# Kernel tuning notes

Hardware: AMD Instinct MI355X
Metric: run time of the kernel (lower is better)

The kernel has to match this reference:

```python
import jax, jax.numpy as jnp
import numpy as np

N, E, P, D = 100000, 800000, 100000, 128

def setup_inputs() -> dict:
    key = jax.random.key(0)
    ks = jax.random.split(key, 24)
    def w(k, i, o):
        return jax.random.normal(k, (i, o), jnp.float32) * (1.0 / np.sqrt(i))
    inp = {
        'x': jax.random.normal(ks[0], (N, D), jnp.float32),
        'src': jax.random.randint(ks[1], (E,), 0, N, jnp.int32),
        'dst': jax.random.randint(ks[2], (E,), 0, N, jnp.int32),
        'pos_src': jax.random.randint(ks[3], (P,), 0, N, jnp.int32),
        'pos_dst': jax.random.randint(ks[4], (P,), 0, N, jnp.int32),
        'neg_src': jax.random.randint(ks[5], (P,), 0, N, jnp.int32),
        'neg_dst': jax.random.randint(ks[6], (P,), 0, N, jnp.int32),
        # SAGEConv params: fc_self, fc_neigh (+bias) per layer
        'Ws0': w(ks[7], D, D), 'Wn0': w(ks[8], D, D), 'b0': jnp.zeros((D,), jnp.float32),
        'Ws1': w(ks[9], D, D), 'Wn1': w(ks[10], D, D), 'b1': jnp.zeros((D,), jnp.float32),
        'Ws2': w(ks[11], D, D), 'Wn2': w(ks[12], D, D), 'b2': jnp.zeros((D,), jnp.float32),
        # predictor MLP: D->D->D->2
        'Wp0': w(ks[13], D, D), 'bp0': jnp.zeros((D,), jnp.float32),
        'Wp1': w(ks[14], D, D), 'bp1': jnp.zeros((D,), jnp.float32),
        'Wp2': w(ks[15], D, 2), 'bp2': jnp.zeros((2,), jnp.float32),
    }
    return inp

def _sage_layer(h, src, dst, n, Ws, Wn, b, act):
    # mean aggregation over in-neighbors (gather -> segment_sum -> divide)
    msum = jax.ops.segment_sum(h[src], dst, num_segments=n)      # [N, D]
    deg = jax.ops.segment_sum(jnp.ones_like(dst, jnp.float32), dst, num_segments=n)
    h_neigh = msum / jnp.maximum(deg, 1.0)[:, None]
    out = h @ Ws + h_neigh @ Wn + b
    return jax.nn.relu(out) if act else out

def _predict(hs, hd, Wp0, bp0, Wp1, bp1, Wp2, bp2):
    z = hs * hd
    z = jax.nn.relu(z @ Wp0 + bp0)
    z = jax.nn.relu(z @ Wp1 + bp1)
    return jax.nn.softmax(z @ Wp2 + bp2, axis=1)[:, 1]

def reference(x, src, dst, pos_src, pos_dst, neg_src, neg_dst,
              Ws0, Wn0, b0, Ws1, Wn1, b1, Ws2, Wn2, b2,
              Wp0, bp0, Wp1, bp1, Wp2, bp2):
    n = x.shape[0]
    h = _sage_layer(x, src, dst, n, Ws0, Wn0, b0, True)
    h = _sage_layer(h, src, dst, n, Ws1, Wn1, b1, True)
    h = _sage_layer(h, src, dst, n, Ws2, Wn2, b2, False)
    pos = _predict(h[pos_src], h[pos_dst], Wp0, bp0, Wp1, bp1, Wp2, bp2)
    neg = _predict(h[neg_src], h[neg_dst], Wp0, bp0, Wp1, bp1, Wp2, bp2)
    return (pos, neg)
```

## Files before the change

kernel.cpp:

```cpp
#include <hip/hip_runtime.h>
#include <cstdint>
#include <cstddef>
#include <cmath>

#define D 128

typedef short bf16x8 __attribute__((ext_vector_type(8)));
typedef float f32x4 __attribute__((ext_vector_type(4)));

__device__ __forceinline__ ushort f2b(float f) {
  uint x = __float_as_uint(f);
  uint r = ((x >> 16) & 1u) + 0x7fffu;
  return (ushort)((x + r) >> 16);
}
__device__ __forceinline__ float b2f(ushort u) {
  return __uint_as_float(((uint)u) << 16);
}

__global__ __launch_bounds__(256) void k_degree_p(const int* __restrict__ dst, int E,
    int* __restrict__ deg, float scale, int CE) {
  int part = blockIdx.x & 7, chunk = blockIdx.x >> 3;
  long base = (long)chunk * CE;
  for (int i = threadIdx.x; i < CE; i += 256) {
    long e = base + i;
    if (e < E) {
      int d = dst[e];
      int p = (int)((float)d * scale); if (p > 7) p = 7;
      if (p == part) atomicAdd(&deg[d], 1);
    }
  }
}

__global__ __launch_bounds__(256) void k_fill_p(const int* __restrict__ src,
    const int* __restrict__ dst, int E, int* __restrict__ cursor,
    int* __restrict__ csrc, float scale, int CE) {
  int part = blockIdx.x & 7, chunk = blockIdx.x >> 3;
  long base = (long)chunk * CE;
  for (int i = threadIdx.x; i < CE; i += 256) {
    long e = base + i;
    if (e < E) {
      int d = dst[e];
      int p = (int)((float)d * scale); if (p > 7) p = 7;
      if (p == part) {
        int s = src[e];
        int pos = atomicAdd(&cursor[d], 1);
        csrc[pos] = s;
      }
    }
  }
}

#define SCAN_T 256
#define SCAN_E 4
#define SCAN_CHUNK (SCAN_T * SCAN_E)

__global__ void k_scan_partial(const int* __restrict__ deg, int n, int* __restrict__ part) {
  __shared__ int s[SCAN_T];
  int base = blockIdx.x * SCAN_CHUNK;
  int sum = 0;
  for (int i = 0; i < SCAN_E; ++i) {
    int idx = base + (int)threadIdx.x * SCAN_E + i;
    if (idx < n) sum += deg[idx];
  }
  s[threadIdx.x] = sum; __syncthreads();
  for (int ofs = SCAN_T / 2; ofs > 0; ofs >>= 1) {
    if ((int)threadIdx.x < ofs) s[threadIdx.x] += s[threadIdx.x + ofs];
    __syncthreads();
  }
  if (threadIdx.x == 0) part[blockIdx.x] = s[0];
}

__global__ void k_scan_part_ex(int* __restrict__ part, int nb) {
  __shared__ int s[1024];
  int v = ((int)threadIdx.x < nb) ? part[threadIdx.x] : 0;
  s[threadIdx.x] = v; __syncthreads();
  for (int ofs = 1; ofs < 1024; ofs <<= 1) {
    int t = ((int)threadIdx.x >= ofs) ? s[threadIdx.x - ofs] : 0;
    __syncthreads();
    s[threadIdx.x] += t;
    __syncthreads();
  }
  if ((int)threadIdx.x < nb) part[threadIdx.x] = s[threadIdx.x] - v;
}

__global__ void k_scan_final(const int* __restrict__ deg, int n, const int* __restrict__ part,
                             int* __restrict__ rowptr, int* __restrict__ cursor, int E) {
  __shared__ int s[SCAN_T];
  int base = blockIdx.x * SCAN_CHUNK;
  int v[SCAN_E]; int local = 0;
  for (int i = 0; i < SCAN_E; ++i) {
    int idx = base + (int)threadIdx.x * SCAN_E + i;
    v[i] = (idx < n) ? deg[idx] : 0;
    local += v[i];
  }
  s[threadIdx.x] = local; __syncthreads();
  for (int ofs = 1; ofs < SCAN_T; ofs <<= 1) {
    int t = ((int)threadIdx.x >= ofs) ? s[threadIdx.x - ofs] : 0;
    __syncthreads();
    s[threadIdx.x] += t;
    __syncthreads();
  }
  int run = part[blockIdx.x] + s[threadIdx.x] - local;
  for (int i = 0; i < SCAN_E; ++i) {
    int idx = base + (int)threadIdx.x * SCAN_E + i;
    if (idx < n) { rowptr[idx] = run; cursor[idx] = run; }
    run += v[i];
  }
  if (blockIdx.x == 0 && threadIdx.x == 0) rowptr[n] = E;
}

__global__ void k_conv_bf16(const float* __restrict__ in, ushort* __restrict__ out, int n8) {
  int i = blockIdx.x * 256 + threadIdx.x;
  if (i >= n8) return;
  float4 a = ((const float4*)in)[i * 2];
  float4 b = ((const float4*)in)[i * 2 + 1];
  ushort4 o0 = {f2b(a.x), f2b(a.y), f2b(a.z), f2b(a.w)};
  ushort4 o1 = {f2b(b.x), f2b(b.y), f2b(b.z), f2b(b.w)};
  ((ushort4*)out)[i * 2] = o0;
  ((ushort4*)out)[i * 2 + 1] = o1;
}

__global__ void k_pack_all(
    const float* __restrict__ Ws0, const float* __restrict__ Wn0,
    const float* __restrict__ Ws1, const float* __restrict__ Wn1,
    const float* __restrict__ Ws2, const float* __restrict__ Wn2,
    const float* __restrict__ Wp0, const float* __restrict__ Wp1,
    ushort* __restrict__ BpL0, ushort* __restrict__ BpL1, ushort* __restrict__ BpL2,
    ushort* __restrict__ BpP0, ushort* __restrict__ BpP1) {
  int o = blockIdx.x * 256 + threadIdx.x;
  const float *W0, *W1; ushort* out; int rel;
  if (o < 32768)       { W0 = Ws0; W1 = Wn0; out = BpL0; rel = o; }
  else if (o < 65536)  { W0 = Ws1; W1 = Wn1; out = BpL1; rel = o - 32768; }
  else if (o < 98304)  { W0 = Ws2; W1 = Wn2; out = BpL2; rel = o - 65536; }
  else if (o < 114688) { W0 = Wp0; W1 = Wp0; out = BpP0; rel = o - 98304; }
  else                 { W0 = Wp1; W1 = Wp1; out = BpP1; rel = o - 114688; }
  int j = rel & 7, lane = (rel >> 3) & 63, t = (rel >> 9) & 7, ks = rel >> 12;
  int k = ks * 32 + ((lane >> 4) * 8) + j;
  int n = t * 16 + (lane & 15);
  const float* W = (k < 128) ? W0 : W1;
  int kk = (k < 128) ? k : k - 128;
  out[rel] = f2b(W[(size_t)kk * D + n]);
}

__global__ __launch_bounds__(256) void k_aggregate2(const ushort* __restrict__ h,
    const int* __restrict__ rowptr, const int* __restrict__ csrc,
    ushort* __restrict__ hn, int N) {
  int tid = threadIdx.x, lane = tid & 63;
  int wid = (int)((blockIdx.x * 256 + tid) >> 6);
  int g = lane >> 4, sub = lane & 15, gb = g << 4;
  int node = wid * 4 + g;
  if (node >= N) return;
  int beg = rowptr[node], end = rowptr[node + 1];
  int dg = end - beg;
  int dd = dg < 16 ? dg : 16;
  int i0 = beg + sub;
  int idxv = (i0 < end) ? csrc[i0] : 0;
  const ushort* hb = h + sub * 8;
  float f[8] = {0.f, 0.f, 0.f, 0.f, 0.f, 0.f, 0.f, 0.f};
  for (int e = 0; e < dd; e += 2) {
    int s0 = __shfl(idxv, gb + e);
    int s1 = __shfl(idxv, gb + e + 1);
    bf16x8 r0 = *(const bf16x8*)(hb + (size_t)s0 * D);
    if (e + 1 < dd) {
      bf16x8 r1 = *(const bf16x8*)(hb + (size_t)s1 * D);
      #pragma unroll
      for (int q = 0; q < 8; ++q)
        f[q] += b2f((ushort)r0[q]) + b2f((ushort)r1[q]);
    } else {
      #pragma unroll
      for (int q = 0; q < 8; ++q) f[q] += b2f((ushort)r0[q]);
    }
  }
  for (int i = beg + 16; i < end; ++i) {
    int s = csrc[i];
    bf16x8 v = *(const bf16x8*)(hb + (size_t)s * D);
    #pragma unroll
    for (int q = 0; q < 8; ++q) f[q] += b2f((ushort)v[q]);
  }
  float inv = (dg > 0) ? (1.0f / (float)dg) : 0.0f;
  bf16x8 o;
  #pragma unroll
  for (int q = 0; q < 8; ++q) o[q] = (short)f2b(f[q] * inv);
  *(bf16x8*)(hn + (size_t)node * D + sub * 8) = o;
}

__global__ __launch_bounds__(256) void k_gemm_mfma(
    const ushort* __restrict__ A, const ushort* __restrict__ An,
    const ushort* __restrict__ Bp, const float* __restrict__ bias,
    ushort* __restrict__ out, int N, int do_relu) {
  int tid = threadIdx.x;
  int wave = tid >> 6, lane = tid & 63;
  int m = lane & 15, kg = lane >> 4;
  int row0 = blockIdx.x * 64 + wave * 16;
  int ar = row0 + m; if (ar >= N) ar = N - 1;
  const ushort* a_self = A  + (size_t)ar * D + kg * 8;
  const ushort* a_nei  = An + (size_t)ar * D + kg * 8;
  f32x4 acc[8];
  #pragma unroll
  for (int t = 0; t < 8; ++t) acc[t] = f32x4{0.f, 0.f, 0.f, 0.f};
  #pragma unroll
  for (int ks = 0; ks < 8; ++ks) {
    const ushort* ap = (ks < 4) ? a_self : a_nei;
    bf16x8 af = *(const bf16x8*)(ap + (ks & 3) * 32);
    const ushort* bb = Bp + (size_t)ks * 4096 + lane * 8;
    #pragma unroll
    for (int t = 0; t < 8; ++t)
      acc[t] = __builtin_amdgcn_mfma_f32_16x16x32_bf16(af, *(const bf16x8*)(bb + t * 512), acc[t], 0, 0, 0);
  }
  #pragma unroll
  for (int t = 0; t < 8; ++t) {
    int c = t * 16 + m;
    float bv = bias[c];
    #pragma unroll
    for (int i = 0; i < 4; ++i) {
      int r = row0 + kg * 4 + i;
      float v = acc[t][i] + bv;
      if (do_relu) v = fmaxf(v, 0.f);
      if (r < N) out[(size_t)r * D + c] = f2b(v);
    }
  }
}

__global__ __launch_bounds__(256) void k_predict_mfma(
    const ushort* __restrict__ h,
    const int* __restrict__ ps, const int* __restrict__ pd,
    const int* __restrict__ ns, const int* __restrict__ nd,
    const ushort* __restrict__ Bp0, const float* __restrict__ bp0,
    const ushort* __restrict__ Bp1, const float* __restrict__ bp1,
    const float* __restrict__ Wp2, const float* __restrict__ bp2,
    float* __restrict__ outp, int P, int pb) {
  __shared__ __align__(16) ushort z1p[4][2048];
  int bi = blockIdx.x;
  const int* sidx; const int* didx; float* op;
  if (bi >= pb) { sidx = ns; didx = nd; op = outp + P; bi -= pb; }
  else          { sidx = ps; didx = pd; op = outp; }
  int tid = threadIdx.x;
  int wave = tid >> 6, lane = tid & 63;
  int m = lane & 15, kg = lane >> 4;
  int pair0 = bi * 64 + wave * 16;
  int prow = pair0 + m; int pr = (prow < P) ? prow : P - 1;
  int si = sidx[pr], di = didx[pr];
  const ushort* hs = h + (size_t)si * D + kg * 8;
  const ushort* hd = h + (size_t)di * D + kg * 8;
  f32x4 acc[8];
  #pragma unroll
  for (int t = 0; t < 8; ++t) acc[t] = f32x4{0.f, 0.f, 0.f, 0.f};
  #pragma unroll
  for (int ks = 0; ks < 4; ++ks) {
    bf16x8 as8 = *(const bf16x8*)(hs + ks * 32);
    bf16x8 ad8 = *(const bf16x8*)(hd + ks * 32);
    bf16x8 af;
    #pragma unroll
    for (int j = 0; j < 8; ++j) {
      float p = b2f((ushort)as8[j]) * b2f((ushort)ad8[j]);
      af[j] = (short)f2b(p);
    }
    const ushort* bb = Bp0 + (size_t)ks * 4096 + lane * 8;
    #pragma unroll
    for (int t = 0; t < 8; ++t)
      acc[t] = __builtin_amdgcn_mfma_f32_16x16x32_bf16(af, *(const bf16x8*)(bb + t * 512), acc[t], 0, 0, 0);
  }
  ushort* zp = &z1p[wave][0];
  #pragma unroll
  for (int t = 0; t < 8; ++t) {
    int c = t * 16 + m;
    float bv = bp0[c];
    int ks2 = c >> 5, kg2 = (c >> 3) & 3, j2 = c & 7;
    #pragma unroll
    for (int i = 0; i < 4; ++i) {
      float v = fmaxf(acc[t][i] + bv, 0.f);
      int l2 = kg2 * 16 + kg * 4 + i;
      zp[(ks2 * 64 + l2) * 8 + j2] = f2b(v);
    }
  }
  __syncthreads();
  #pragma unroll
  for (int t = 0; t < 8; ++t) acc[t] = f32x4{0.f, 0.f, 0.f, 0.f};
  #pragma unroll
  for (int ks = 0; ks < 4; ++ks) {
    bf16x8 af = *(const bf16x8*)(zp + (ks * 64 + lane) * 8);
    const ushort* bb = Bp1 + (size_t)ks * 4096 + lane * 8;
    #pragma unroll
    for (int t = 0; t < 8; ++t)
      acc[t] = __builtin_amdgcn_mfma_f32_16x16x32_bf16(af, *(const bf16x8*)(bb + t * 512), acc[t], 0, 0, 0);
  }
  float p0[4] = {0.f, 0.f, 0.f, 0.f}, p1[4] = {0.f, 0.f, 0.f, 0.f};
  #pragma unroll
  for (int t = 0; t < 8; ++t) {
    int c = t * 16 + m;
    float bv = bp1[c];
    float wa = Wp2[(size_t)c * 2], wb = Wp2[(size_t)c * 2 + 1];
    #pragma unroll
    for (int i = 0; i < 4; ++i) {
      float z = fmaxf(acc[t][i] + bv, 0.f);
      p0[i] += z * wa;
      p1[i] += z * wb;
    }
  }
  #pragma unroll
  for (int msk = 1; msk <= 8; msk <<= 1) {
    #pragma unroll
    for (int i = 0; i < 4; ++i) {
      p0[i] += __shfl_xor(p0[i], msk);
      p1[i] += __shfl_xor(p1[i], msk);
    }
  }
  if (m == 0) {
    float c0 = bp2[0], c1 = bp2[1];
    #pragma unroll
    for (int i = 0; i < 4; ++i) {
      int r = pair0 + kg * 4 + i;
      if (r < P) {
        float l0 = p0[i] + c0, l1 = p1[i] + c1;
        op[r] = 1.0f / (1.0f + expf(l0 - l1));
      }
    }
  }
}

extern "C" void kernel_launch(void* const* d_in, const int* in_sizes, int n_in,
                              void* d_out, int out_size, void* d_ws, size_t ws_size,
                              hipStream_t stream) {
  const float* x       = (const float*)d_in[0];
  const int*   src     = (const int*)d_in[1];
  const int*   dst     = (const int*)d_in[2];
  const int*   pos_src = (const int*)d_in[3];
  const int*   pos_dst = (const int*)d_in[4];
  const int*   neg_src = (const int*)d_in[5];
  const int*   neg_dst = (const int*)d_in[6];
  const float* Ws0 = (const float*)d_in[7],  *Wn0 = (const float*)d_in[8],  *b0 = (const float*)d_in[9];
  const float* Ws1 = (const float*)d_in[10], *Wn1 = (const float*)d_in[11], *b1 = (const float*)d_in[12];
  const float* Ws2 = (const float*)d_in[13], *Wn2 = (const float*)d_in[14], *b2 = (const float*)d_in[15];
  const float* Wp0 = (const float*)d_in[16], *bp0 = (const float*)d_in[17];
  const float* Wp1 = (const float*)d_in[18], *bp1 = (const float*)d_in[19];
  const float* Wp2 = (const float*)d_in[20], *bp2 = (const float*)d_in[21];
  const int N = in_sizes[0] / D;
  const int E = in_sizes[1];
  const int P = in_sizes[3];
  float* outp = (float*)d_out;

  char* ws = (char*)d_ws;
  size_t off = 0;
  auto alloc = [&](size_t bytes) -> void* {
    void* p = ws + off;
    off += (bytes + 255) & ~(size_t)255;
    return p;
  };
  ushort* xb    = (ushort*)alloc((size_t)N * D * 2);
  ushort* h1    = (ushort*)alloc((size_t)N * D * 2);
  ushort* h2    = (ushort*)alloc((size_t)N * D * 2);
  ushort* hn    = (ushort*)alloc((size_t)N * D * 2);
  ushort* BpL0  = (ushort*)alloc(256 * D * 2);
  ushort* BpL1  = (ushort*)alloc(256 * D * 2);
  ushort* BpL2  = (ushort*)alloc(256 * D * 2);
  ushort* BpP0  = (ushort*)alloc(128 * D * 2);
  ushort* BpP1  = (ushort*)alloc(128 * D * 2);
  int*    deg    = (int*)alloc((size_t)N * 4);
  int*    rowptr = (int*)alloc((size_t)(N + 1) * 4);
  int*    cursor = (int*)alloc((size_t)N * 4);
  int*    part   = (int*)alloc(4096);
  int*    csrc   = (int*)alloc((size_t)E * 4);
  (void)ws_size; (void)n_in; (void)out_size;

  const float pscale = 8.0f / (float)N;
  const int CB = 96;
  const int CE = (E + CB - 1) / CB;

  hipMemsetAsync(deg, 0, (size_t)N * 4, stream);
  k_degree_p<<<8 * CB, 256, 0, stream>>>(dst, E, deg, pscale, CE);
  int nb = (N + SCAN_CHUNK - 1) / SCAN_CHUNK;
  k_scan_partial<<<nb, SCAN_T, 0, stream>>>(deg, N, part);
  k_scan_part_ex<<<1, 1024, 0, stream>>>(part, nb);
  k_scan_final<<<nb, SCAN_T, 0, stream>>>(deg, N, part, rowptr, cursor, E);
  k_fill_p<<<8 * CB, 256, 0, stream>>>(src, dst, E, cursor, csrc, pscale, CE);

  int n8 = N * D / 8;
  k_conv_bf16<<<(n8 + 255) / 256, 256, 0, stream>>>(x, xb, n8);
  k_pack_all<<<512, 256, 0, stream>>>(Ws0, Wn0, Ws1, Wn1, Ws2, Wn2, Wp0, Wp1,
                                      BpL0, BpL1, BpL2, BpP0, BpP1);

  int aggb = (N + 15) / 16;
  int gemb = (N + 63) / 64;
  k_aggregate2<<<aggb, 256, 0, stream>>>(xb, rowptr, csrc, hn, N);
  k_gemm_mfma<<<gemb, 256, 0, stream>>>(xb, hn, BpL0, b0, h1, N, 1);
  k_aggregate2<<<aggb, 256, 0, stream>>>(h1, rowptr, csrc, hn, N);
  k_gemm_mfma<<<gemb, 256, 0, stream>>>(h1, hn, BpL1, b1, h2, N, 1);
  k_aggregate2<<<aggb, 256, 0, stream>>>(h2, rowptr, csrc, hn, N);
  k_gemm_mfma<<<gemb, 256, 0, stream>>>(h2, hn, BpL2, b2, xb, N, 0);

  int pb = (P + 63) / 64;
  k_predict_mfma<<<2 * pb, 256, 0, stream>>>(xb, pos_src, pos_dst, neg_src, neg_dst,
                                             BpP0, bp0, BpP1, bp1, Wp2, bp2, outp, P, pb);
}
```

Measured before the change: 463.8 us.

## Fuse prep kernels, unroll aggregation by four, swizzle predictor LDS layout

Merges the degree memset, x-to-bf16 conversion and weight packing into a single grid-stride prep kernel, removing two launches and one memset. The aggregation loop now issues up to four neighbour row loads per iteration instead of two, giving more memory-level parallelism. The predictor's shared-memory staging for the second layer uses a permuted lane index to reduce bank conflicts on the writes. The fused prep kernel uses only 512 blocks for the large conversion, which may underuse bandwidth compared with the old one-thread-per-element launch.

```diff
diff --git a/kernel.cpp b/kernel.cpp
--- a/kernel.cpp
+++ b/kernel.cpp
@@ -15,6 +15,46 @@
 }
 __device__ __forceinline__ float b2f(ushort u) {
   return __uint_as_float(((uint)u) << 16);
+}
+__device__ __forceinline__ int pis(int l) {
+  return (l & 0x20) | ((l & 3) << 3) | (((l >> 4) & 1) << 2) | ((l >> 2) & 3);
+}
+
+__global__ __launch_bounds__(256) void k_prep(
+    const float* __restrict__ x, ushort* __restrict__ xb,
+    const float* __restrict__ Ws0, const float* __restrict__ Wn0,
+    const float* __restrict__ Ws1, const float* __restrict__ Wn1,
+    const float* __restrict__ Ws2, const float* __restrict__ Wn2,
+    const float* __restrict__ Wp0, const float* __restrict__ Wp1,
+    ushort* __restrict__ BpL0, ushort* __restrict__ BpL1, ushort* __restrict__ BpL2,
+    ushort* __restrict__ BpP0, ushort* __restrict__ BpP1,
+    int* __restrict__ deg, int N) {
+  int TOTg = gridDim.x * 256;
+  int gtid = blockIdx.x * 256 + threadIdx.x;
+  for (int i = gtid; i < N; i += TOTg) deg[i] = 0;
+  int n8 = N * (D / 8);
+  const float4* xin = (const float4*)x;
+  for (int i = gtid; i < n8; i += TOTg) {
+    float4 a = xin[i * 2], b = xin[i * 2 + 1];
+    ushort4 o0 = {f2b(a.x), f2b(a.y), f2b(a.z), f2b(a.w)};
+    ushort4 o1 = {f2b(b.x), f2b(b.y), f2b(b.z), f2b(b.w)};
+    ((ushort4*)xb)[i * 2] = o0;
+    ((ushort4*)xb)[i * 2 + 1] = o1;
+  }
+  for (int o = gtid; o < 131072; o += TOTg) {
+    const float *W0, *W1; ushort* outw; int rel;
+    if (o < 32768)       { W0 = Ws0; W1 = Wn0; outw = BpL0; rel = o; }
+    else if (o < 65536)  { W0 = Ws1; W1 = Wn1; outw = BpL1; rel = o - 32768; }
+    else if (o < 98304)  { W0 = Ws2; W1 = Wn2; outw = BpL2; rel = o - 65536; }
+    else if (o < 114688) { W0 = Wp0; W1 = Wp0; outw = BpP0; rel = o - 98304; }
+    else                 { W0 = Wp1; W1 = Wp1; outw = BpP1; rel = o - 114688; }
+    int j = rel & 7, lane = (rel >> 3) & 63, t = (rel >> 9) & 7, ks = rel >> 12;
+    int k = ks * 32 + ((lane >> 4) * 8) + j;
+    int n = t * 16 + (lane & 15);
+    const float* W = (k < 128) ? W0 : W1;
+    int kk = (k < 128) ? k : k - 128;
+    outw[rel] = f2b(W[(size_t)kk * D + n]);
+  }
 }
 
 __global__ __launch_bounds__(256) void k_degree_p(const int* __restrict__ dst, int E,
@@ -109,39 +149,6 @@
   if (blockIdx.x == 0 && threadIdx.x == 0) rowptr[n] = E;
 }
 
-__global__ void k_conv_bf16(const float* __restrict__ in, ushort* __restrict__ out, int n8) {
-  int i = blockIdx.x * 256 + threadIdx.x;
-  if (i >= n8) return;
-  float4 a = ((const float4*)in)[i * 2];
-  float4 b = ((const float4*)in)[i * 2 + 1];
-  ushort4 o0 = {f2b(a.x), f2b(a.y), f2b(a.z), f2b(a.w)};
-  ushort4 o1 = {f2b(b.x), f2b(b.y), f2b(b.z), f2b(b.w)};
-  ((ushort4*)out)[i * 2] = o0;
-  ((ushort4*)out)[i * 2 + 1] = o1;
-}
-
-__global__ void k_pack_all(
-    const float* __restrict__ Ws0, const float* __restrict__ Wn0,
-    const float* __restrict__ Ws1, const float* __restrict__ Wn1,
-    const float* __restrict__ Ws2, const float* __restrict__ Wn2,
-    const float* __restrict__ Wp0, const float* __restrict__ Wp1,
-    ushort* __restrict__ BpL0, ushort* __restrict__ BpL1, ushort* __restrict__ BpL2,
-    ushort* __restrict__ BpP0, ushort* __restrict__ BpP1) {
-  int o = blockIdx.x * 256 + threadIdx.x;
-  const float *W0, *W1; ushort* out; int rel;
-  if (o < 32768)       { W0 = Ws0; W1 = Wn0; out = BpL0; rel = o; }
-  else if (o < 65536)  { W0 = Ws1; W1 = Wn1; out = BpL1; rel = o - 32768; }
-  else if (o < 98304)  { W0 = Ws2; W1 = Wn2; out = BpL2; rel = o - 65536; }
-  else if (o < 114688) { W0 = Wp0; W1 = Wp0; out = BpP0; rel = o - 98304; }
-  else                 { W0 = Wp1; W1 = Wp1; out = BpP1; rel = o - 114688; }
-  int j = rel & 7, lane = (rel >> 3) & 63, t = (rel >> 9) & 7, ks = rel >> 12;
-  int k = ks * 32 + ((lane >> 4) * 8) + j;
-  int n = t * 16 + (lane & 15);
-  const float* W = (k < 128) ? W0 : W1;
-  int kk = (k < 128) ? k : k - 128;
-  out[rel] = f2b(W[(size_t)kk * D + n]);
-}
-
 __global__ __launch_bounds__(256) void k_aggregate2(const ushort* __restrict__ h,
     const int* __restrict__ rowptr, const int* __restrict__ csrc,
     ushort* __restrict__ hn, int N) {
@@ -157,15 +164,33 @@
   int idxv = (i0 < end) ? csrc[i0] : 0;
   const ushort* hb = h + sub * 8;
   float f[8] = {0.f, 0.f, 0.f, 0.f, 0.f, 0.f, 0.f, 0.f};
-  for (int e = 0; e < dd; e += 2) {
+  for (int e = 0; e < dd; e += 4) {
     int s0 = __shfl(idxv, gb + e);
     int s1 = __shfl(idxv, gb + e + 1);
+    int s2 = __shfl(idxv, gb + e + 2);
+    int s3 = __shfl(idxv, gb + e + 3);
+    int cnt = dd - e;
     bf16x8 r0 = *(const bf16x8*)(hb + (size_t)s0 * D);
-    if (e + 1 < dd) {
+    if (cnt > 1) {
       bf16x8 r1 = *(const bf16x8*)(hb + (size_t)s1 * D);
-      #pragma unroll
-      for (int q = 0; q < 8; ++q)
-        f[q] += b2f((ushort)r0[q]) + b2f((ushort)r1[q]);
+      if (cnt > 2) {
+        bf16x8 r2 = *(const bf16x8*)(hb + (size_t)s2 * D);
+        if (cnt > 3) {
+          bf16x8 r3 = *(const bf16x8*)(hb + (size_t)s3 * D);
+          #pragma unroll
+          for (int q = 0; q < 8; ++q)
+            f[q] += (b2f((ushort)r0[q]) + b2f((ushort)r1[q]))
+                  + (b2f((ushort)r2[q]) + b2f((ushort)r3[q]));
+        } else {
+          #pragma unroll
+          for (int q = 0; q < 8; ++q)
+            f[q] += b2f((ushort)r0[q]) + b2f((ushort)r1[q]) + b2f((ushort)r2[q]);
+        }
+      } else {
+        #pragma unroll
+        for (int q = 0; q < 8; ++q)
+          f[q] += b2f((ushort)r0[q]) + b2f((ushort)r1[q]);
+      }
     } else {
       #pragma unroll
       for (int q = 0; q < 8; ++q) f[q] += b2f((ushort)r0[q]);
@@ -237,6 +262,7 @@
   int tid = threadIdx.x;
   int wave = tid >> 6, lane = tid & 63;
   int m = lane & 15, kg = lane >> 4;
+  int pl = pis(lane);
   int pair0 = bi * 64 + wave * 16;
   int prow = pair0 + m; int pr = (prow < P) ? prow : P - 1;
   int si = sidx[pr], di = didx[pr];
@@ -270,7 +296,7 @@
     for (int i = 0; i < 4; ++i) {
       float v = fmaxf(acc[t][i] + bv, 0.f);
       int l2 = kg2 * 16 + kg * 4 + i;
-      zp[(ks2 * 64 + l2) * 8 + j2] = f2b(v);
+      zp[ks2 * 512 + pis(l2) * 8 + j2] = f2b(v);
     }
   }
   __syncthreads();
@@ -278,7 +304,7 @@
   for (int t = 0; t < 8; ++t) acc[t] = f32x4{0.f, 0.f, 0.f, 0.f};
   #pragma unroll
   for (int ks = 0; ks < 4; ++ks) {
-    bf16x8 af = *(const bf16x8*)(zp + (ks * 64 + lane) * 8);
+    bf16x8 af = *(const bf16x8*)(zp + ks * 512 + pl * 8);
     const ushort* bb = Bp1 + (size_t)ks * 4096 + lane * 8;
     #pragma unroll
     for (int t = 0; t < 8; ++t)
@@ -366,18 +392,14 @@
   const int CB = 96;
   const int CE = (E + CB - 1) / CB;
 
-  hipMemsetAsync(deg, 0, (size_t)N * 4, stream);
+  k_prep<<<512, 256, 0, stream>>>(x, xb, Ws0, Wn0, Ws1, Wn1, Ws2, Wn2, Wp0, Wp1,
+                                  BpL0, BpL1, BpL2, BpP0, BpP1, deg, N);
   k_degree_p<<<8 * CB, 256, 0, stream>>>(dst, E, deg, pscale, CE);
   int nb = (N + SCAN_CHUNK - 1) / SCAN_CHUNK;
   k_scan_partial<<<nb, SCAN_T, 0, stream>>>(deg, N, part);
   k_scan_part_ex<<<1, 1024, 0, stream>>>(part, nb);
   k_scan_final<<<nb, SCAN_T, 0, stream>>>(deg, N, part, rowptr, cursor, E);
   k_fill_p<<<8 * CB, 256, 0, stream>>>(src, dst, E, cursor, csrc, pscale, CE);
-
-  int n8 = N * D / 8;
-  k_conv_bf16<<<(n8 + 255) / 256, 256, 0, stream>>>(x, xb, n8);
-  k_pack_all<<<512, 256, 0, stream>>>(Ws0, Wn0, Ws1, Wn1, Ws2, Wn2, Wp0, Wp1,
-                                      BpL0, BpL1, BpL2, BpP0, BpP1);
 
   int aggb = (N + 15) / 16;
   int gemb = (N + 63) / 64;
```

Result: no change. 467.5 us (+0.8%).
